# Performance work log

Hardware: AMD Instinct MI355X
Metric: run time of the kernel (lower is better)

Reference implementation:

```python
import jax, jax.numpy as jnp
import numpy as np

N_NODES = 100000
N_EDGES = 1600000


def _tconv(x, src, dst, Wq, bq, Wk, bk, Wv, bv, Ws, bs):
    """PyG TransformerConv (heads=1, concat=True, root_weight=True), eval mode."""
    n = x.shape[0]
    q = x @ Wq + bq          # [N, d]
    k = x @ Wk + bk
    v = x @ Wv + bv
    scale = 1.0 / jnp.sqrt(jnp.asarray(q.shape[1], q.dtype))
    # per-edge attention logits: query at destination, key at source
    alpha = jnp.sum(q[dst] * k[src], axis=-1) * scale       # [E]
    # segment softmax over incoming edges of each destination node
    m = jax.ops.segment_max(alpha, dst, num_segments=n)      # [N]
    e = jnp.exp(alpha - m[dst])
    s = jax.ops.segment_sum(e, dst, num_segments=n)          # [N]
    a = e / s[dst]                                           # [E]
    agg = jax.ops.segment_sum(a[:, None] * v[src], dst, num_segments=n)  # [N, d]
    return agg + x @ Ws + bs  # skip connection (root_weight=True)


def setup_inputs() -> dict:
    key = jax.random.key(0)
    ks = jax.random.split(key, 20)
    x = jax.random.normal(ks[0], (N_NODES, 2), dtype=jnp.float32)
    edge_index = jax.random.randint(ks[1], (2, N_EDGES), 0, N_NODES, dtype=jnp.int64)
    def lin(k, din, dout):
        k1, k2 = jax.random.split(k)
        lim = 1.0 / np.sqrt(din)
        W = jax.random.uniform(k1, (din, dout), jnp.float32, -lim, lim)
        b = jax.random.uniform(k2, (dout,), jnp.float32, -lim, lim)
        return W, b
    Wq1, bq1 = lin(ks[2], 2, 256)
    Wk1, bk1 = lin(ks[3], 2, 256)
    Wv1, bv1 = lin(ks[4], 2, 256)
    Ws1, bs1 = lin(ks[5], 2, 256)
    Wq2, bq2 = lin(ks[6], 256, 2)
    Wk2, bk2 = lin(ks[7], 256, 2)
    Wv2, bv2 = lin(ks[8], 256, 2)
    Ws2, bs2 = lin(ks[9], 256, 2)
    return dict(x=x, edge_index=edge_index,
                Wq1=Wq1, bq1=bq1, Wk1=Wk1, bk1=bk1, Wv1=Wv1, bv1=bv1, Ws1=Ws1, bs1=bs1,
                Wq2=Wq2, bq2=bq2, Wk2=Wk2, bk2=bk2, Wv2=Wv2, bv2=bv2, Ws2=Ws2, bs2=bs2)


def reference(x, edge_index,
              Wq1, bq1, Wk1, bk1, Wv1, bv1, Ws1, bs1,
              Wq2, bq2, Wk2, bk2, Wv2, bv2, Ws2, bs2):
    src, dst = edge_index[0], edge_index[1]
    h = _tconv(x, src, dst, Wq1, bq1, Wk1, bk1, Wv1, bv1, Ws1, bs1)
    h = jax.nn.relu(h)
    # F.dropout is identity in eval mode
    h = _tconv(h, src, dst, Wq2, bq2, Wk2, bk2, Wv2, bv2, Ws2, bs2)
    return jax.nn.log_softmax(h, axis=1)
```

## Files before the change

kernel.cpp:

```cpp
#include <hip/hip_runtime.h>


#define R_LOG2   8
#define R_DSTS   256
#define BE       4096
#define MAXNB    512
#define RSQRT2   0.70710678118654752f

__device__ __forceinline__ int wave_excl_scan(int v, int lane, int& total) {
    int incl = v;
#pragma unroll
    for (int o = 1; o < 64; o <<= 1) {
        int t = __shfl_up(incl, o);
        if (lane >= o) incl += t;
    }
    total = __shfl(incl, 63);
    return incl - v;
}

__global__ void coeff_k(const float* __restrict__ Wq1, const float* __restrict__ bq1,
                        const float* __restrict__ Wk1, const float* __restrict__ bk1,
                        float* __restrict__ coeff) {
    __shared__ float part[4][9];
    int c = threadIdx.x;
    float wq0 = Wq1[c], wq1 = Wq1[256 + c];
    float wk0 = Wk1[c], wk1 = Wk1[256 + c];
    float bq = bq1[c], bk = bk1[c];
    float vals[9] = { wq0 * wk0, wq0 * wk1, wq1 * wk0, wq1 * wk1,
                      wq0 * bk,  wq1 * bk,  bq * wk0,  bq * wk1,  bq * bk };
    int lane = c & 63, w = c >> 6;
#pragma unroll
    for (int i = 0; i < 9; ++i) {
        float v = vals[i];
#pragma unroll
        for (int o = 32; o > 0; o >>= 1) v += __shfl_xor(v, o);
        if (lane == 0) part[w][i] = v;
    }
    __syncthreads();
    if (c < 9) coeff[c] = part[0][c] + part[1][c] + part[2][c] + part[3][c];
}

__global__ __launch_bounds__(256) void count_k(
        const int* __restrict__ dst, int* __restrict__ C,
        int NB, int NBlk, int E) {
    __shared__ int hist[MAXNB];
    int t = threadIdx.x;
    for (int i = t; i < NB; i += 256) hist[i] = 0;
    __syncthreads();
    int base = blockIdx.x * BE;
    int nloc = E - base; if (nloc > BE) nloc = BE;
    int nv = nloc >> 2;
    const int4* d4 = (const int4*)(dst + base);
    for (int i = t; i < nv; i += 256) {
        int4 v = d4[i];
        atomicAdd(&hist[v.x >> R_LOG2], 1);
        atomicAdd(&hist[v.y >> R_LOG2], 1);
        atomicAdd(&hist[v.z >> R_LOG2], 1);
        atomicAdd(&hist[v.w >> R_LOG2], 1);
    }
    for (int i = (nv << 2) + t; i < nloc; i += 256)
        atomicAdd(&hist[dst[base + i] >> R_LOG2], 1);
    __syncthreads();
    for (int b = t; b < NB; b += 256)
        C[(size_t)b * NBlk + blockIdx.x] = hist[b];
}

__global__ __launch_bounds__(256) void rowscan_k(
        int* __restrict__ C, int* __restrict__ rowTotal, int NB, int NBlk) {
    int lane = threadIdx.x & 63;
    int row = blockIdx.x * 4 + (threadIdx.x >> 6);
    if (row >= NB) return;
    int carry = 0;
    for (int j0 = 0; j0 < NBlk; j0 += 64) {
        int idx = j0 + lane;
        int v = (idx < NBlk) ? C[(size_t)row * NBlk + idx] : 0;
        int tot, ex = wave_excl_scan(v, lane, tot);
        if (idx < NBlk) C[(size_t)row * NBlk + idx] = ex + carry;
        carry += tot;
    }
    if (lane == 0) rowTotal[row] = carry;
}

__global__ __launch_bounds__(64) void bucketscan_k(
        const int* __restrict__ rowTotal, int* __restrict__ bucketBase, int NB) {
    int lane = threadIdx.x;
    int carry = 0;
    for (int j0 = 0; j0 < NB; j0 += 64) {
        int idx = j0 + lane;
        int v = (idx < NB) ? rowTotal[idx] : 0;
        int tot, ex = wave_excl_scan(v, lane, tot);
        if (idx < NB) bucketBase[idx] = ex + carry;
        carry += tot;
    }
    if (lane == 0) bucketBase[NB] = carry;
}

__global__ __launch_bounds__(256) void scatter2_k(
        const int* __restrict__ src, const int* __restrict__ dst,
        const int* __restrict__ C, const int* __restrict__ bucketBase,
        int* __restrict__ recs, int NB, int NBlk, int E) {
    __shared__ int hist[MAXNB];
    __shared__ int lofs[MAXNB];
    __shared__ int gbase[MAXNB];
    __shared__ int stage[BE];
    __shared__ unsigned short sbkt[BE];
    __shared__ int wsum[4];
    int t = threadIdx.x;
    for (int i = t; i < NB; i += 256) hist[i] = 0;
    __syncthreads();

    int blk = blockIdx.x;
    int base = blk * BE;
    int nloc = E - base; if (nloc > BE) nloc = BE;
    int nv = nloc >> 2;
    const int4* d4 = (const int4*)(dst + base);
    const int4* s4 = (const int4*)(src + base);

    for (int i = t; i < nv; i += 256) {
        int4 v = d4[i];
        atomicAdd(&hist[v.x >> R_LOG2], 1);
        atomicAdd(&hist[v.y >> R_LOG2], 1);
        atomicAdd(&hist[v.z >> R_LOG2], 1);
        atomicAdd(&hist[v.w >> R_LOG2], 1);
    }
    for (int i = (nv << 2) + t; i < nloc; i += 256)
        atomicAdd(&hist[dst[base + i] >> R_LOG2], 1);
    __syncthreads();

    {
        int i0 = 2 * t, i1 = 2 * t + 1;
        int a = (i0 < NB) ? hist[i0] : 0;
        int b = (i1 < NB) ? hist[i1] : 0;
        int s = a + b;
        int lane = t & 63, w = t >> 6;
        int incl = s;
#pragma unroll
        for (int o = 1; o < 64; o <<= 1) {
            int u = __shfl_up(incl, o);
            if (lane >= o) incl += u;
        }
        if (lane == 63) wsum[w] = incl;
        __syncthreads();
        int ex = incl - s;
        for (int j = 0; j < w; ++j) ex += wsum[j];
        if (i0 < NB) lofs[i0] = ex;
        if (i1 < NB) lofs[i1] = ex + a;
    }
    __syncthreads();

    for (int b = t; b < NB; b += 256) {
        gbase[b] = bucketBase[b] + C[(size_t)b * NBlk + blk] - lofs[b];
        hist[b] = 0;
    }
    __syncthreads();

    for (int i = t; i < nv; i += 256) {
        int4 dv = d4[i];
        int4 sv = s4[i];
        int d, b, r, p;
        d = dv.x; b = d >> R_LOG2; r = atomicAdd(&hist[b], 1); p = lofs[b] + r;
        stage[p] = sv.x | ((d & (R_DSTS - 1)) << 17); sbkt[p] = (unsigned short)b;
        d = dv.y; b = d >> R_LOG2; r = atomicAdd(&hist[b], 1); p = lofs[b] + r;
        stage[p] = sv.y | ((d & (R_DSTS - 1)) << 17); sbkt[p] = (unsigned short)b;
        d = dv.z; b = d >> R_LOG2; r = atomicAdd(&hist[b], 1); p = lofs[b] + r;
        stage[p] = sv.z | ((d & (R_DSTS - 1)) << 17); sbkt[p] = (unsigned short)b;
        d = dv.w; b = d >> R_LOG2; r = atomicAdd(&hist[b], 1); p = lofs[b] + r;
        stage[p] = sv.w | ((d & (R_DSTS - 1)) << 17); sbkt[p] = (unsigned short)b;
    }
    for (int i = (nv << 2) + t; i < nloc; i += 256) {
        int d = dst[base + i];
        int b = d >> R_LOG2;
        int r = atomicAdd(&hist[b], 1);
        int p = lofs[b] + r;
        stage[p] = src[base + i] | ((d & (R_DSTS - 1)) << 17);
        sbkt[p] = (unsigned short)b;
    }
    __syncthreads();

    for (int i = t; i < nloc; i += 256)
        recs[gbase[sbkt[i]] + i] = stage[i];
}

__global__ __launch_bounds__(256) void l1f_k(
        const float* __restrict__ x, const float* __restrict__ coeff,
        const int* __restrict__ recs, const int* __restrict__ bucketBase,
        const float* __restrict__ Wv1, const float* __restrict__ bv1,
        const float* __restrict__ Ws1, const float* __restrict__ bs1,
        const float* __restrict__ Wq2, const float* __restrict__ bq2,
        const float* __restrict__ Wk2, const float* __restrict__ bk2,
        const float* __restrict__ Wv2, const float* __restrict__ bv2,
        const float* __restrict__ Ws2, const float* __restrict__ bs2,
        float* __restrict__ q2, float4* __restrict__ kv2,
        float* __restrict__ hs2, int N) {
    __shared__ float sW[14][256];
    __shared__ float p0[R_DSTS], p1[R_DSTS], pc[R_DSTS];
    __shared__ float ac0[R_DSTS], ac1[R_DSTS], ac2[R_DSTS];
    int t = threadIdx.x;
    sW[0][t]  = Wv1[t];
    sW[1][t]  = Wv1[256 + t];
    sW[2][t]  = Ws1[t];
    sW[3][t]  = Ws1[256 + t];
    sW[4][t]  = bv1[t];
    sW[5][t]  = bs1[t];
    sW[6][t]  = Wq2[2 * t];
    sW[7][t]  = Wq2[2 * t + 1];
    sW[8][t]  = Wk2[2 * t];
    sW[9][t]  = Wk2[2 * t + 1];
    sW[10][t] = Wv2[2 * t];
    sW[11][t] = Wv2[2 * t + 1];
    sW[12][t] = Ws2[2 * t];
    sW[13][t] = Ws2[2 * t + 1];

    int b = blockIdx.x;
    int nbase = b << R_LOG2;
    int rem = N - nbase; if (rem > R_DSTS) rem = R_DSTS;

    ac0[t] = 0.f; ac1[t] = 0.f; ac2[t] = 0.f;
    float2 xd = make_float2(0.f, 0.f);
    if (t < rem) {
        xd = ((const float2*)x)[nbase + t];
        float c0 = coeff[0], c1 = coeff[1], c2 = coeff[2], c3 = coeff[3];
        float c4 = coeff[4], c5 = coeff[5], c6 = coeff[6], c7 = coeff[7];
        float c8 = coeff[8];
        p0[t] = c0 * xd.x + c2 * xd.y + c6;
        p1[t] = c1 * xd.x + c3 * xd.y + c7;
        pc[t] = c4 * xd.x + c5 * xd.y + c8;
    }
    __syncthreads();

    int eb = bucketBase[b], ee = bucketBase[b + 1];
    for (int i = eb + t; i < ee; i += 256) {
        int rec = recs[i];
        int s = rec & 0x1FFFF;
        int dl = (rec >> 17) & (R_DSTS - 1);
        float2 xs = ((const float2*)x)[s];
        float w = __expf((p0[dl] * xs.x + p1[dl] * xs.y + pc[dl]) * 0.0625f);
        atomicAdd(&ac0[dl], w);
        atomicAdd(&ac1[dl], w * xs.x);
        atomicAdd(&ac2[dl], w * xs.y);
    }
    __syncthreads();

    if (t >= rem) return;
    float s = ac0[t];
    float a0 = 0.f, a1 = 0.f, he = 0.f;
    if (s > 0.f) {
        float inv = 1.0f / s;
        a0 = ac1[t] * inv; a1 = ac2[t] * inv; he = 1.f;
    }

    float acc0 = 0.f, acc1 = 0.f, acc2 = 0.f, acc3 = 0.f;
    float acc4 = 0.f, acc5 = 0.f, acc6 = 0.f, acc7 = 0.f;
#pragma unroll 8
    for (int c = 0; c < 256; ++c) {
        float h = a0 * sW[0][c] + a1 * sW[1][c]
                + xd.x * sW[2][c] + xd.y * sW[3][c]
                + he * sW[4][c] + sW[5][c];
        h = fmaxf(h, 0.f);
        acc0 += h * sW[6][c];
        acc1 += h * sW[7][c];
        acc2 += h * sW[8][c];
        acc3 += h * sW[9][c];
        acc4 += h * sW[10][c];
        acc5 += h * sW[11][c];
        acc6 += h * sW[12][c];
        acc7 += h * sW[13][c];
    }
    int n = nbase + t;
    ((float2*)q2)[n]  = make_float2(acc0 + bq2[0], acc1 + bq2[1]);
    kv2[n] = make_float4(acc2 + bk2[0], acc3 + bk2[1],
                         acc4 + bv2[0], acc5 + bv2[1]);
    ((float2*)hs2)[n] = make_float2(acc6 + bs2[0], acc7 + bs2[1]);
}

__global__ __launch_bounds__(256) void l2f_k(
        const float* __restrict__ q2, const float4* __restrict__ kv2,
        const float* __restrict__ hs2,
        const int* __restrict__ recs, const int* __restrict__ bucketBase,
        float* __restrict__ out, int N) {
    __shared__ float qx[R_DSTS], qy[R_DSTS];
    __shared__ float ac0[R_DSTS], ac1[R_DSTS], ac2[R_DSTS];
    int t = threadIdx.x;
    int b = blockIdx.x;
    int nbase = b << R_LOG2;
    int rem = N - nbase; if (rem > R_DSTS) rem = R_DSTS;

    ac0[t] = 0.f; ac1[t] = 0.f; ac2[t] = 0.f;
    if (t < rem) {
        float2 q = ((const float2*)q2)[nbase + t];
        qx[t] = q.x * RSQRT2;
        qy[t] = q.y * RSQRT2;
    }
    __syncthreads();

    int eb = bucketBase[b], ee = bucketBase[b + 1];
    for (int i = eb + t; i < ee; i += 256) {
        int rec = recs[i];
        int s = rec & 0x1FFFF;
        int dl = (rec >> 17) & (R_DSTS - 1);
        float4 kv = kv2[s];
        float w = __expf(qx[dl] * kv.x + qy[dl] * kv.y);
        atomicAdd(&ac0[dl], w);
        atomicAdd(&ac1[dl], w * kv.z);
        atomicAdd(&ac2[dl], w * kv.w);
    }
    __syncthreads();

    if (t >= rem) return;
    float s = ac0[t];
    float g0 = 0.f, g1 = 0.f;
    if (s > 0.f) {
        float inv = 1.0f / s;
        g0 = ac1[t] * inv; g1 = ac2[t] * inv;
    }
    int n = nbase + t;
    float2 hs = ((const float2*)hs2)[n];
    float o0 = g0 + hs.x;
    float o1 = g1 + hs.y;
    float mx = fmaxf(o0, o1), mn = fminf(o0, o1);
    float lse = mx + log1pf(__expf(mn - mx));
    ((float2*)out)[n] = make_float2(o0 - lse, o1 - lse);
}

extern "C" void kernel_launch(void* const* d_in, const int* in_sizes, int n_in,
                              void* d_out, int out_size, void* d_ws, size_t ws_size,
                              hipStream_t stream) {
    const float* x   = (const float*)d_in[0];
    const int*   ei  = (const int*)d_in[1];
    const float* Wq1 = (const float*)d_in[2];
    const float* bq1 = (const float*)d_in[3];
    const float* Wk1 = (const float*)d_in[4];
    const float* bk1 = (const float*)d_in[5];
    const float* Wv1 = (const float*)d_in[6];
    const float* bv1 = (const float*)d_in[7];
    const float* Ws1 = (const float*)d_in[8];
    const float* bs1 = (const float*)d_in[9];
    const float* Wq2 = (const float*)d_in[10];
    const float* bq2 = (const float*)d_in[11];
    const float* Wk2 = (const float*)d_in[12];
    const float* bk2 = (const float*)d_in[13];
    const float* Wv2 = (const float*)d_in[14];
    const float* bv2 = (const float*)d_in[15];
    const float* Ws2 = (const float*)d_in[16];
    const float* bs2 = (const float*)d_in[17];

    const int N = in_sizes[0] / 2;
    const int E = in_sizes[1] / 2;
    const int* src = ei;
    const int* dst = ei + E;

    const int NB   = (N + R_DSTS - 1) >> R_LOG2;
    const int NBlk = (E + BE - 1) / BE;

    float* ws = (float*)d_ws;
    size_t off = 0;
    float* coeff      = ws + off;            off += 16;
    int*   bucketBase = (int*)(ws + off);    off += (size_t)NB + 1;
    int*   rowTotal   = (int*)(ws + off);    off += NB;
    int*   C          = (int*)(ws + off);    off += (size_t)NB * NBlk;
    int*   recs       = (int*)(ws + off);    off += E;
    off = (off + 3) & ~(size_t)3;
    float4* kv2       = (float4*)(ws + off); off += 4 * (size_t)N;
    float* q2         = ws + off;            off += 2 * (size_t)N;
    float* hs2        = ws + off;            off += 2 * (size_t)N;

    const int gN = (N + 255) / 256;
    (void)gN;

    coeff_k<<<1, 256, 0, stream>>>(Wq1, bq1, Wk1, bk1, coeff);
    count_k<<<NBlk, 256, 0, stream>>>(dst, C, NB, NBlk, E);
    rowscan_k<<<(NB + 3) / 4, 256, 0, stream>>>(C, rowTotal, NB, NBlk);
    bucketscan_k<<<1, 64, 0, stream>>>(rowTotal, bucketBase, NB);
    scatter2_k<<<NBlk, 256, 0, stream>>>(src, dst, C, bucketBase, recs, NB, NBlk, E);
    l1f_k<<<NB, 256, 0, stream>>>(x, coeff, recs, bucketBase,
                                  Wv1, bv1, Ws1, bs1,
                                  Wq2, bq2, Wk2, bk2, Wv2, bv2, Ws2, bs2,
                                  q2, kv2, hs2, N);
    l2f_k<<<NB, 256, 0, stream>>>(q2, kv2, hs2, recs, bucketBase, (float*)d_out, N);
}
```

Measured before the change: 126.6 us.

## Split per-bucket edge reductions into slices with separate node finalize kernels

Each destination bucket's edge range is split across 8 blocks that write partial softmax sums to a workspace buffer. Separate node-level kernels then reduce the partials and do the dense MLP and the final log-softmax. The aim is more parallelism than NB≈391 blocks gives on a GPU with many CUs, so the gather and atomic phase is spread across more of the device. In exchange it adds two kernel launches and partial-sum traffic, and node_k now reads weights from global memory instead of staging them in LDS.

```diff
diff --git a/kernel.cpp b/kernel.cpp
--- a/kernel.cpp
+++ b/kernel.cpp
@@ -5,6 +5,7 @@
 #define R_DSTS   256
 #define BE       4096
 #define MAXNB    512
+#define S_SLICES 8
 #define RSQRT2   0.70710678118654752f
 
 __device__ __forceinline__ int wave_excl_scan(int v, int lane, int& total) {
@@ -181,9 +182,55 @@
         recs[gbase[sbkt[i]] + i] = stage[i];
 }
 
-__global__ __launch_bounds__(256) void l1f_k(
+__global__ __launch_bounds__(256) void l1r_k(
         const float* __restrict__ x, const float* __restrict__ coeff,
         const int* __restrict__ recs, const int* __restrict__ bucketBase,
+        float* __restrict__ part, int N) {
+    __shared__ float p0[R_DSTS], p1[R_DSTS], pc[R_DSTS];
+    __shared__ float ac[3 * R_DSTS];
+    int t = threadIdx.x;
+    int bs = blockIdx.x;
+    int b = bs / S_SLICES;
+    int sl = bs - b * S_SLICES;
+    int nbase = b << R_LOG2;
+    int rem = N - nbase; if (rem > R_DSTS) rem = R_DSTS;
+
+    ac[t] = 0.f; ac[256 + t] = 0.f; ac[512 + t] = 0.f;
+    if (t < rem) {
+        float2 xd = ((const float2*)x)[nbase + t];
+        float c0 = coeff[0], c1 = coeff[1], c2 = coeff[2], c3 = coeff[3];
+        float c4 = coeff[4], c5 = coeff[5], c6 = coeff[6], c7 = coeff[7];
+        float c8 = coeff[8];
+        p0[t] = c0 * xd.x + c2 * xd.y + c6;
+        p1[t] = c1 * xd.x + c3 * xd.y + c7;
+        pc[t] = c4 * xd.x + c5 * xd.y + c8;
+    }
+    __syncthreads();
+
+    int eb = bucketBase[b], ee = bucketBase[b + 1];
+    int len = (ee - eb + S_SLICES - 1) / S_SLICES;
+    int lo = eb + sl * len;
+    int hi = lo + len; if (hi > ee) hi = ee;
+    for (int i = lo + t; i < hi; i += 256) {
+        int rec = recs[i];
+        int s = rec & 0x1FFFF;
+        int dl = (rec >> 17) & (R_DSTS - 1);
+        float2 xs = ((const float2*)x)[s];
+        float w = __expf((p0[dl] * xs.x + p1[dl] * xs.y + pc[dl]) * 0.0625f);
+        atomicAdd(&ac[dl], w);
+        atomicAdd(&ac[256 + dl], w * xs.x);
+        atomicAdd(&ac[512 + dl], w * xs.y);
+    }
+    __syncthreads();
+
+    float* dp = part + (size_t)bs * (3 * R_DSTS);
+    dp[t] = ac[t];
+    dp[256 + t] = ac[256 + t];
+    dp[512 + t] = ac[512 + t];
+}
+
+__global__ __launch_bounds__(256) void node_k(
+        const float* __restrict__ x, const float* __restrict__ part,
         const float* __restrict__ Wv1, const float* __restrict__ bv1,
         const float* __restrict__ Ws1, const float* __restrict__ bs1,
         const float* __restrict__ Wq2, const float* __restrict__ bq2,
@@ -192,100 +239,64 @@
         const float* __restrict__ Ws2, const float* __restrict__ bs2,
         float* __restrict__ q2, float4* __restrict__ kv2,
         float* __restrict__ hs2, int N) {
-    __shared__ float sW[14][256];
-    __shared__ float p0[R_DSTS], p1[R_DSTS], pc[R_DSTS];
-    __shared__ float ac0[R_DSTS], ac1[R_DSTS], ac2[R_DSTS];
-    int t = threadIdx.x;
-    sW[0][t]  = Wv1[t];
-    sW[1][t]  = Wv1[256 + t];
-    sW[2][t]  = Ws1[t];
-    sW[3][t]  = Ws1[256 + t];
-    sW[4][t]  = bv1[t];
-    sW[5][t]  = bs1[t];
-    sW[6][t]  = Wq2[2 * t];
-    sW[7][t]  = Wq2[2 * t + 1];
-    sW[8][t]  = Wk2[2 * t];
-    sW[9][t]  = Wk2[2 * t + 1];
-    sW[10][t] = Wv2[2 * t];
-    sW[11][t] = Wv2[2 * t + 1];
-    sW[12][t] = Ws2[2 * t];
-    sW[13][t] = Ws2[2 * t + 1];
-
+    int t = threadIdx.x;
     int b = blockIdx.x;
-    int nbase = b << R_LOG2;
-    int rem = N - nbase; if (rem > R_DSTS) rem = R_DSTS;
-
-    ac0[t] = 0.f; ac1[t] = 0.f; ac2[t] = 0.f;
-    float2 xd = make_float2(0.f, 0.f);
-    if (t < rem) {
-        xd = ((const float2*)x)[nbase + t];
-        float c0 = coeff[0], c1 = coeff[1], c2 = coeff[2], c3 = coeff[3];
-        float c4 = coeff[4], c5 = coeff[5], c6 = coeff[6], c7 = coeff[7];
-        float c8 = coeff[8];
-        p0[t] = c0 * xd.x + c2 * xd.y + c6;
-        p1[t] = c1 * xd.x + c3 * xd.y + c7;
-        pc[t] = c4 * xd.x + c5 * xd.y + c8;
-    }
-    __syncthreads();
-
-    int eb = bucketBase[b], ee = bucketBase[b + 1];
-    for (int i = eb + t; i < ee; i += 256) {
-        int rec = recs[i];
-        int s = rec & 0x1FFFF;
-        int dl = (rec >> 17) & (R_DSTS - 1);
-        float2 xs = ((const float2*)x)[s];
-        float w = __expf((p0[dl] * xs.x + p1[dl] * xs.y + pc[dl]) * 0.0625f);
-        atomicAdd(&ac0[dl], w);
-        atomicAdd(&ac1[dl], w * xs.x);
-        atomicAdd(&ac2[dl], w * xs.y);
-    }
-    __syncthreads();
-
-    if (t >= rem) return;
-    float s = ac0[t];
+    int n = (b << R_LOG2) + t;
+    if (n >= N) return;
+
+    const float* pp = part + (size_t)b * S_SLICES * (3 * R_DSTS);
+    float s = 0.f, sx0 = 0.f, sx1 = 0.f;
+#pragma unroll
+    for (int sl = 0; sl < S_SLICES; ++sl) {
+        s   += pp[sl * 768 + t];
+        sx0 += pp[sl * 768 + 256 + t];
+        sx1 += pp[sl * 768 + 512 + t];
+    }
+
     float a0 = 0.f, a1 = 0.f, he = 0.f;
     if (s > 0.f) {
         float inv = 1.0f / s;
-        a0 = ac1[t] * inv; a1 = ac2[t] * inv; he = 1.f;
-    }
+        a0 = sx0 * inv; a1 = sx1 * inv; he = 1.f;
+    }
+    float2 xd = ((const float2*)x)[n];
 
     float acc0 = 0.f, acc1 = 0.f, acc2 = 0.f, acc3 = 0.f;
     float acc4 = 0.f, acc5 = 0.f, acc6 = 0.f, acc7 = 0.f;
 #pragma unroll 8
     for (int c = 0; c < 256; ++c) {
-        float h = a0 * sW[0][c] + a1 * sW[1][c]
-                + xd.x * sW[2][c] + xd.y * sW[3][c]
-                + he * sW[4][c] + sW[5][c];
+        float h = a0 * Wv1[c] + a1 * Wv1[256 + c]
+                + xd.x * Ws1[c] + xd.y * Ws1[256 + c]
+                + he * bv1[c] + bs1[c];
         h = fmaxf(h, 0.f);
-        acc0 += h * sW[6][c];
-        acc1 += h * sW[7][c];
-        acc2 += h * sW[8][c];
-        acc3 += h * sW[9][c];
-        acc4 += h * sW[10][c];
-        acc5 += h * sW[11][c];
-        acc6 += h * sW[12][c];
-        acc7 += h * sW[13][c];
-    }
-    int n = nbase + t;
+        acc0 += h * Wq2[2 * c];
+        acc1 += h * Wq2[2 * c + 1];
+        acc2 += h * Wk2[2 * c];
+        acc3 += h * Wk2[2 * c + 1];
+        acc4 += h * Wv2[2 * c];
+        acc5 += h * Wv2[2 * c + 1];
+        acc6 += h * Ws2[2 * c];
+        acc7 += h * Ws2[2 * c + 1];
+    }
     ((float2*)q2)[n]  = make_float2(acc0 + bq2[0], acc1 + bq2[1]);
     kv2[n] = make_float4(acc2 + bk2[0], acc3 + bk2[1],
                          acc4 + bv2[0], acc5 + bv2[1]);
     ((float2*)hs2)[n] = make_float2(acc6 + bs2[0], acc7 + bs2[1]);
 }
 
-__global__ __launch_bounds__(256) void l2f_k(
+__global__ __launch_bounds__(256) void l2r_k(
         const float* __restrict__ q2, const float4* __restrict__ kv2,
-        const float* __restrict__ hs2,
         const int* __restrict__ recs, const int* __restrict__ bucketBase,
-        float* __restrict__ out, int N) {
+        float* __restrict__ part, int N) {
     __shared__ float qx[R_DSTS], qy[R_DSTS];
-    __shared__ float ac0[R_DSTS], ac1[R_DSTS], ac2[R_DSTS];
-    int t = threadIdx.x;
-    int b = blockIdx.x;
+    __shared__ float ac[3 * R_DSTS];
+    int t = threadIdx.x;
+    int bs = blockIdx.x;
+    int b = bs / S_SLICES;
+    int sl = bs - b * S_SLICES;
     int nbase = b << R_LOG2;
     int rem = N - nbase; if (rem > R_DSTS) rem = R_DSTS;
 
-    ac0[t] = 0.f; ac1[t] = 0.f; ac2[t] = 0.f;
+    ac[t] = 0.f; ac[256 + t] = 0.f; ac[512 + t] = 0.f;
     if (t < rem) {
         float2 q = ((const float2*)q2)[nbase + t];
         qx[t] = q.x * RSQRT2;
@@ -294,26 +305,48 @@
     __syncthreads();
 
     int eb = bucketBase[b], ee = bucketBase[b + 1];
-    for (int i = eb + t; i < ee; i += 256) {
+    int len = (ee - eb + S_SLICES - 1) / S_SLICES;
+    int lo = eb + sl * len;
+    int hi = lo + len; if (hi > ee) hi = ee;
+    for (int i = lo + t; i < hi; i += 256) {
         int rec = recs[i];
         int s = rec & 0x1FFFF;
         int dl = (rec >> 17) & (R_DSTS - 1);
         float4 kv = kv2[s];
         float w = __expf(qx[dl] * kv.x + qy[dl] * kv.y);
-        atomicAdd(&ac0[dl], w);
-        atomicAdd(&ac1[dl], w * kv.z);
-        atomicAdd(&ac2[dl], w * kv.w);
-    }
-    __syncthreads();
-
-    if (t >= rem) return;
-    float s = ac0[t];
+        atomicAdd(&ac[dl], w);
+        atomicAdd(&ac[256 + dl], w * kv.z);
+        atomicAdd(&ac[512 + dl], w * kv.w);
+    }
+    __syncthreads();
+
+    float* dp = part + (size_t)bs * (3 * R_DSTS);
+    dp[t] = ac[t];
+    dp[256 + t] = ac[256 + t];
+    dp[512 + t] = ac[512 + t];
+}
+
+__global__ __launch_bounds__(256) void out2_k(
+        const float* __restrict__ part, const float* __restrict__ hs2,
+        float* __restrict__ out, int N) {
+    int t = threadIdx.x;
+    int b = blockIdx.x;
+    int n = (b << R_LOG2) + t;
+    if (n >= N) return;
+
+    const float* pp = part + (size_t)b * S_SLICES * (3 * R_DSTS);
+    float s = 0.f, sv0 = 0.f, sv1 = 0.f;
+#pragma unroll
+    for (int sl = 0; sl < S_SLICES; ++sl) {
+        s   += pp[sl * 768 + t];
+        sv0 += pp[sl * 768 + 256 + t];
+        sv1 += pp[sl * 768 + 512 + t];
+    }
     float g0 = 0.f, g1 = 0.f;
     if (s > 0.f) {
         float inv = 1.0f / s;
-        g0 = ac1[t] * inv; g1 = ac2[t] * inv;
-    }
-    int n = nbase + t;
+        g0 = sv0 * inv; g1 = sv1 * inv;
+    }
     float2 hs = ((const float2*)hs2)[n];
     float o0 = g0 + hs.x;
     float o1 = g1 + hs.y;
@@ -360,21 +393,20 @@
     int*   C          = (int*)(ws + off);    off += (size_t)NB * NBlk;
     int*   recs       = (int*)(ws + off);    off += E;
     off = (off + 3) & ~(size_t)3;
+    float* part       = ws + off;            off += (size_t)NB * S_SLICES * 3 * R_DSTS;
     float4* kv2       = (float4*)(ws + off); off += 4 * (size_t)N;
     float* q2         = ws + off;            off += 2 * (size_t)N;
     float* hs2        = ws + off;            off += 2 * (size_t)N;
-
-    const int gN = (N + 255) / 256;
-    (void)gN;
 
     coeff_k<<<1, 256, 0, stream>>>(Wq1, bq1, Wk1, bk1, coeff);
     count_k<<<NBlk, 256, 0, stream>>>(dst, C, NB, NBlk, E);
     rowscan_k<<<(NB + 3) / 4, 256, 0, stream>>>(C, rowTotal, NB, NBlk);
     bucketscan_k<<<1, 64, 0, stream>>>(rowTotal, bucketBase, NB);
     scatter2_k<<<NBlk, 256, 0, stream>>>(src, dst, C, bucketBase, recs, NB, NBlk, E);
-    l1f_k<<<NB, 256, 0, stream>>>(x, coeff, recs, bucketBase,
-                                  Wv1, bv1, Ws1, bs1,
-                                  Wq2, bq2, Wk2, bk2, Wv2, bv2, Ws2, bs2,
-                                  q2, kv2, hs2, N);
-    l2f_k<<<NB, 256, 0, stream>>>(q2, kv2, hs2, recs, bucketBase, (float*)d_out, N);
-}
+    l1r_k<<<NB * S_SLICES, 256, 0, stream>>>(x, coeff, recs, bucketBase, part, N);
+    node_k<<<NB, 256, 0, stream>>>(x, part, Wv1, bv1, Ws1, bs1,
+                                   Wq2, bq2, Wk2, bk2, Wv2, bv2, Ws2, bs2,
+                                   q2, kv2, hs2, N);
+    l2r_k<<<NB * S_SLICES, 256, 0, stream>>>(q2, kv2, recs, bucketBase, part, N);
+    out2_k<<<NB, 256, 0, stream>>>(part, hs2, (float*)d_out, N);
+}
```

New measurement: 135.2 us. +6.8%, slower.
